# Kernel tuning notes

Hardware: AMD Instinct MI355X
Metric: run time of the kernel (lower is better)

Reference implementation:

```python
import jax, jax.numpy as jnp
import numpy as np

N_HEADS = 16

def setup_inputs() -> dict:
    key = jax.random.key(0)
    ks = jax.random.split(key, 7)
    B, S, D = 2, 2048, 1024
    sc = 0.02
    return {
        "x": jax.random.normal(ks[0], (B, S, D), dtype=jnp.float32),
        "Wq": jax.random.normal(ks[1], (D, D), dtype=jnp.float32) * sc,
        "bq": jax.random.normal(ks[2], (D,), dtype=jnp.float32) * sc,
        "Wk": jax.random.normal(ks[3], (D, D), dtype=jnp.float32) * sc,
        "bk": jax.random.normal(ks[4], (D,), dtype=jnp.float32) * sc,
        "Wv": jax.random.normal(ks[5], (D, D), dtype=jnp.float32) * sc,
        "bv": jax.random.normal(ks[6], (D,), dtype=jnp.float32) * sc,
    }

def reference(x, Wq, bq, Wk, bk, Wv, bv):
    B, S, D = x.shape
    H = N_HEADS
    W = D // H  # head width
    # torch Linear: y = x @ W.T + b
    q = x @ Wq.T + bq
    k = x @ Wk.T + bk
    v = x @ Wv.T + bv
    # split last dim into (H, W) and move heads forward: (B, H, S, W)
    q = q.reshape(B, S, H, W).transpose(0, 2, 1, 3)
    k = k.reshape(B, S, H, W).transpose(0, 2, 1, 3)
    v = v.reshape(B, S, H, W).transpose(0, 2, 1, 3)
    scores = jnp.einsum("bhqw,bhkw->bhqk", q, k) / jnp.sqrt(jnp.asarray(W, x.dtype))
    # original applies softmax, (dropout=identity at eval), then softmax AGAIN
    scores = jax.nn.softmax(scores, axis=-1)
    scores = jax.nn.softmax(scores, axis=-1)
    h = jnp.einsum("bhqk,bhkw->bhqw", scores, v)
    h = h.transpose(0, 2, 1, 3).reshape(B, S, D)
    return h
```

## Files before the change

kernel.cpp:

```cpp
#include <hip/hip_runtime.h>
#include <cstdint>
#include <cstddef>

typedef __bf16 bf16_t;
typedef __bf16 bf16x2 __attribute__((ext_vector_type(2)));
typedef __bf16 bf16x4 __attribute__((ext_vector_type(4)));
typedef __bf16 bf16x8 __attribute__((ext_vector_type(8)));
typedef float f32x4 __attribute__((ext_vector_type(4)));
typedef unsigned int u32x2 __attribute__((ext_vector_type(2)));

typedef __attribute__((address_space(1))) unsigned int gu32;
typedef __attribute__((address_space(3))) unsigned int lu32;

#define MFMA16(a, b, c) __builtin_amdgcn_mfma_f32_16x16x32_bf16((a), (b), (c), 0, 0, 0)

__device__ __forceinline__ void gload_lds16(const void* g, void* l) {
    __builtin_amdgcn_global_load_lds((gu32*)const_cast<void*>(g), (lu32*)l, 16, 0, 0);
}

__global__ __launch_bounds__(256) void cvt_bf16(
    const float* __restrict__ x, const float* __restrict__ Wq,
    const float* __restrict__ Wk, const float* __restrict__ Wv,
    bf16_t* __restrict__ xb, bf16_t* __restrict__ Wqb,
    bf16_t* __restrict__ Wkb, bf16_t* __restrict__ Wvb)
{
    const int z = blockIdx.z;
    const float* src = (z == 0) ? x : (z == 1) ? Wq : (z == 2) ? Wk : Wv;
    bf16_t* dst      = (z == 0) ? xb : (z == 1) ? Wqb : (z == 2) ? Wkb : Wvb;
    const int n = (z == 0) ? 4096 * 1024 : 1024 * 1024;
    const int stride = gridDim.x * blockDim.x * 4;
    for (int i = (blockIdx.x * blockDim.x + threadIdx.x) * 4; i < n; i += stride) {
        const float4 f = *(const float4*)(src + i);
        bf16x4 o; o[0] = (bf16_t)f.x; o[1] = (bf16_t)f.y; o[2] = (bf16_t)f.z; o[3] = (bf16_t)f.w;
        *(bf16x4*)(dst + i) = o;
    }
}

__global__ __launch_bounds__(512) void qkv_gemm_bf16(
    const bf16_t* __restrict__ xb,
    const bf16_t* __restrict__ W0b, const float* __restrict__ b0,
    const bf16_t* __restrict__ W1b, const float* __restrict__ b1,
    const bf16_t* __restrict__ W2b, const float* __restrict__ b2,
    bf16_t* __restrict__ Qo, bf16_t* __restrict__ Ko, bf16_t* __restrict__ VTo,
    float* __restrict__ Vp)
{
    const int z = blockIdx.z;
    const bf16_t* Wm = (z == 0) ? W0b : (z == 1) ? W1b : W2b;
    const float* bia = (z == 0) ? b0 : (z == 1) ? b1 : b2;

    __shared__ bf16_t As[2][128 * 32];
    __shared__ bf16_t Bs[2][128 * 32];

    const int tid  = threadIdx.x;
    const int lane = tid & 63;
    const int wv   = tid >> 6;
    const int quad = lane >> 4;
    const int l16  = lane & 15;
    const int wm   = wv >> 1;
    const int wn   = wv & 1;
    const int m0   = blockIdx.x * 128;
    const int n0   = blockIdx.y * 128;

    const int rs = tid >> 2;
    const int gs = ((tid & 3) ^ ((rs >> 1) & 3)) * 8;
    const int fp = (quad ^ ((l16 >> 1) & 3)) * 8;

    f32x4 acc[2][4];
    for (int i = 0; i < 2; i++)
        for (int j = 0; j < 4; j++) acc[i][j] = (f32x4)0.0f;

    gload_lds16(xb + (size_t)(m0 + rs) * 1024 + gs, &As[0][(wv * 64) * 8]);
    gload_lds16(Wm + (size_t)(n0 + rs) * 1024 + gs, &Bs[0][(wv * 64) * 8]);

#pragma unroll 2
    for (int kt = 0; kt < 32; kt++) {
        const int cur = kt & 1, nxt = cur ^ 1;
        __syncthreads();
        if (kt < 31) {
            const int kp = (kt + 1) * 32;
            gload_lds16(xb + (size_t)(m0 + rs) * 1024 + kp + gs, &As[nxt][(wv * 64) * 8]);
            gload_lds16(Wm + (size_t)(n0 + rs) * 1024 + kp + gs, &Bs[nxt][(wv * 64) * 8]);
        }
        bf16x8 af[2], bfr[4];
        for (int mt = 0; mt < 2; mt++)
            af[mt] = *(const bf16x8*)&As[cur][(wm * 32 + mt * 16 + l16) * 32 + fp];
        for (int nt = 0; nt < 4; nt++)
            bfr[nt] = *(const bf16x8*)&Bs[cur][(wn * 64 + nt * 16 + l16) * 32 + fp];
        for (int mt = 0; mt < 2; mt++)
            for (int nt = 0; nt < 4; nt++)
                acc[mt][nt] = MFMA16(af[mt], bfr[nt], acc[mt][nt]);
    }

    float bv[4];
    for (int nt = 0; nt < 4; nt++)
        bv[nt] = bia[n0 + wn * 64 + nt * 16 + l16];

    if (z < 2) {
        bf16_t* out = (z == 0) ? Qo : Ko;
        const float scl = (z == 0) ? 0.18033688011112042f : 1.0f;
        for (int mt = 0; mt < 2; mt++) {
            const int mrow = m0 + wm * 32 + mt * 16 + quad * 4;
            for (int nt = 0; nt < 4; nt++) {
                const int n = n0 + wn * 64 + nt * 16 + l16;
                for (int r = 0; r < 4; r++)
                    out[(size_t)(mrow + r) * 1024 + n] = (bf16_t)((acc[mt][nt][r] + bv[nt]) * scl);
            }
        }
    } else {
        const int h = blockIdx.y * 2 + wn;
        float psum[4] = {0.f, 0.f, 0.f, 0.f};
        for (int mt = 0; mt < 2; mt++) {
            const int sg = m0 + wm * 32 + mt * 16 + quad * 4;
            const int bb = sg >> 11;
            const int s  = sg & 2047;
            for (int nt = 0; nt < 4; nt++) {
                const int w = nt * 16 + l16;
                bf16x4 pk;
                for (int r = 0; r < 4; r++) {
                    pk[r] = (bf16_t)(acc[mt][nt][r] + bv[nt]);
                    psum[nt] += (float)pk[r];
                }
                *(bf16x4*)(VTo + ((size_t)((bb * 16 + h) * 64 + w)) * 2048 + s) = pk;
            }
        }
        for (int nt = 0; nt < 4; nt++) {
            psum[nt] += __shfl_xor(psum[nt], 16, 64);
            psum[nt] += __shfl_xor(psum[nt], 32, 64);
        }
        float* red = (float*)&As[0][0];
        if (quad == 0)
            for (int nt = 0; nt < 4; nt++)
                red[(wv * 4 + nt) * 16 + l16] = psum[nt];
        __syncthreads();
        if (wm == 0 && quad == 0) {
            const int bb = m0 >> 11;
            const int j  = blockIdx.x & 15;
            for (int nt = 0; nt < 4; nt++) {
                float s4 = ((red[((wn + 0) * 4 + nt) * 16 + l16]
                           + red[((wn + 2) * 4 + nt) * 16 + l16])
                           + red[((wn + 4) * 4 + nt) * 16 + l16])
                           + red[((wn + 6) * 4 + nt) * 16 + l16];
                Vp[((size_t)((bb * 16 + h) * 64 + nt * 16 + l16)) * 16 + j] = s4;
            }
        }
    }
}

__global__ __launch_bounds__(512, 4) void attn(
    const bf16_t* __restrict__ Qg, const bf16_t* __restrict__ Kg,
    const bf16_t* __restrict__ VTg, const float* __restrict__ Vp,
    float* __restrict__ out)
{
    const int qt = blockIdx.x;
    const int h  = blockIdx.y;
    const int b  = blockIdx.z;

    const int tid  = threadIdx.x;
    const int wv   = tid >> 6;
    const int lane = tid & 63;
    const int quad = lane >> 4;
    const int l16  = lane & 15;
    const int qg   = wv >> 1;
    const int sh   = wv & 1;

    const size_t base  = ((size_t)b * 2048) * 1024 + (size_t)h * 64;
    const size_t vbase = ((size_t)(b * 16 + h) * 64) * 2048;
    const int q0 = qt * 128;

    __shared__ __align__(16) unsigned char smem[49152];
    bf16_t* Qs = (bf16_t*)smem;

    {
        const int c0 = tid, c1 = 512 + tid;
        const int r0 = c0 >> 3, g0 = ((c0 & 7) ^ (r0 & 7)) * 8;
        const int r1 = c1 >> 3, g1 = ((c1 & 7) ^ (r1 & 7)) * 8;
        gload_lds16(Qg + base + (size_t)(q0 + r0) * 1024 + g0, Qs + (wv * 64) * 8);
        gload_lds16(Qg + base + (size_t)(q0 + r1) * 1024 + g1, Qs + (512 + wv * 64) * 8);
    }
    const int rk = tid >> 3;
    const int gk = ((tid & 7) ^ (rk & 7)) * 8;
    gload_lds16(Kg + base + (size_t)rk * 1024 + gk,
                (bf16_t*)(smem + 16384) + (wv * 64) * 8);
    gload_lds16(VTg + vbase + (size_t)rk * 2048 + gk,
                (bf16_t*)(smem + 32768) + (wv * 64) * 8);

    const int fs0 = ((0 ^ quad) ^ (l16 & 7)) * 8;
    const int fs1 = ((4 ^ quad) ^ (l16 & 7)) * 8;
    const int fsA = sh ? fs1 : fs0;

    const int qr0 = qg * 32 + l16;
    const int qr1 = qg * 32 + 16 + l16;

    f32x4 oa[2][4], l1acc[2];
    for (int qs = 0; qs < 2; qs++) {
        for (int nt = 0; nt < 4; nt++) oa[qs][nt] = (f32x4)0.0f;
        l1acc[qs] = (f32x4)0.0f;
    }

    bf16x8 ones;
    for (int j = 0; j < 8; j++) ones[j] = (bf16_t)1.0f;

    __syncthreads();

    bf16x8 aq[2][2];
    aq[0][0] = *(const bf16x8*)&Qs[qr0 * 64 + fs0];
    aq[0][1] = *(const bf16x8*)&Qs[qr0 * 64 + fs1];
    aq[1][0] = *(const bf16x8*)&Qs[qr1 * 64 + fs0];
    aq[1][1] = *(const bf16x8*)&Qs[qr1 * 64 + fs1];

    bf16x8 af[2];
    bf16x8 bvf[4];

    #define EXCHANGE_P(PS_SA)                                                   \
        for (int qs = 0; qs < 2; qs++) {                                        \
            union { bf16x2 h; unsigned int u; } t00, t01, t10, t11;             \
            t00.h[0] = (bf16_t)__builtin_amdgcn_exp2f(PS_SA[0][qs][0]);         \
            t00.h[1] = (bf16_t)__builtin_amdgcn_exp2f(PS_SA[0][qs][1]);         \
            t01.h[0] = (bf16_t)__builtin_amdgcn_exp2f(PS_SA[0][qs][2]);         \
            t01.h[1] = (bf16_t)__builtin_amdgcn_exp2f(PS_SA[0][qs][3]);         \
            t10.h[0] = (bf16_t)__builtin_amdgcn_exp2f(PS_SA[1][qs][0]);         \
            t10.h[1] = (bf16_t)__builtin_amdgcn_exp2f(PS_SA[1][qs][1]);         \
            t11.h[0] = (bf16_t)__builtin_amdgcn_exp2f(PS_SA[1][qs][2]);         \
            t11.h[1] = (bf16_t)__builtin_amdgcn_exp2f(PS_SA[1][qs][3]);         \
            u32x2 p0 = __builtin_amdgcn_permlane32_swap(t00.u, t10.u, false, false); \
            u32x2 e0 = __builtin_amdgcn_permlane16_swap(p0[0], p0[1], false, false); \
            u32x2 p1 = __builtin_amdgcn_permlane32_swap(t01.u, t11.u, false, false); \
            u32x2 e1 = __builtin_amdgcn_permlane16_swap(p1[0], p1[1], false, false); \
            union { unsigned int u[4]; bf16x8 h; } w;                           \
            w.u[0] = e0[0]; w.u[1] = e1[0]; w.u[2] = e0[1]; w.u[3] = e1[1];     \
            af[qs] = w.h;                                                       \
        }

    {
        const bf16_t* Ks0 = (const bf16_t*)(smem + 16384);
        const bf16_t* Vs0 = (const bf16_t*)(smem + 32768);
        gload_lds16(Kg + base + (size_t)(64 + rk) * 1024 + gk,
                    (bf16_t*)(smem + 24576) + (wv * 64) * 8);
        gload_lds16(VTg + vbase + (size_t)rk * 2048 + 64 + gk,
                    (bf16_t*)(smem + 40960) + (wv * 64) * 8);

        f32x4 sa[2][2];
        for (int st = 0; st < 2; st++)
            for (int qs = 0; qs < 2; qs++) sa[st][qs] = (f32x4)0.0f;
        for (int st = 0; st < 2; st++) {
            const int srow = (sh * 32 + st * 16 + l16) * 64;
            bf16x8 kb0 = *(const bf16x8*)&Ks0[srow + fs0];
            bf16x8 kb1 = *(const bf16x8*)&Ks0[srow + fs1];
            for (int qs = 0; qs < 2; qs++) {
                sa[st][qs] = MFMA16(kb0, aq[qs][0], sa[st][qs]);
                sa[st][qs] = MFMA16(kb1, aq[qs][1], sa[st][qs]);
            }
        }
        EXCHANGE_P(sa)
        for (int nt = 0; nt < 4; nt++)
            bvf[nt] = *(const bf16x8*)&Vs0[(nt * 16 + l16) * 64 + fsA];
    }

#pragma unroll 2
    for (int kt = 1; kt < 32; kt++) {
        const int cur = kt & 1, prv = cur ^ 1;
        const bf16_t* KsC = (const bf16_t*)(smem + 16384 + cur * 8192);
        const bf16_t* VsC = (const bf16_t*)(smem + 32768 + cur * 8192);
        __syncthreads();

        if (kt < 31) {
            gload_lds16(Kg + base + (size_t)((kt + 1) * 64 + rk) * 1024 + gk,
                        (bf16_t*)(smem + 16384 + prv * 8192) + (wv * 64) * 8);
            gload_lds16(VTg + vbase + (size_t)rk * 2048 + (kt + 1) * 64 + gk,
                        (bf16_t*)(smem + 32768 + prv * 8192) + (wv * 64) * 8);
        }

        f32x4 sa[2][2];
        for (int st = 0; st < 2; st++)
            for (int qs = 0; qs < 2; qs++) sa[st][qs] = (f32x4)0.0f;
        __builtin_amdgcn_s_setprio(1);
        for (int st = 0; st < 2; st++) {
            const int srow = (sh * 32 + st * 16 + l16) * 64;
            bf16x8 kb0 = *(const bf16x8*)&KsC[srow + fs0];
            bf16x8 kb1 = *(const bf16x8*)&KsC[srow + fs1];
            for (int qs = 0; qs < 2; qs++) {
                sa[st][qs] = MFMA16(kb0, aq[qs][0], sa[st][qs]);
                sa[st][qs] = MFMA16(kb1, aq[qs][1], sa[st][qs]);
            }
        }

        l1acc[0] = MFMA16(af[0], ones, l1acc[0]);
        l1acc[1] = MFMA16(af[1], ones, l1acc[1]);
        for (int nt = 0; nt < 4; nt++) {
            oa[0][nt] = MFMA16(af[0], bvf[nt], oa[0][nt]);
            oa[1][nt] = MFMA16(af[1], bvf[nt], oa[1][nt]);
        }
        __builtin_amdgcn_s_setprio(0);

        for (int nt = 0; nt < 4; nt++)
            bvf[nt] = *(const bf16x8*)&VsC[(nt * 16 + l16) * 64 + fsA];

        EXCHANGE_P(sa)
    }

    {
        l1acc[0] = MFMA16(af[0], ones, l1acc[0]);
        l1acc[1] = MFMA16(af[1], ones, l1acc[1]);
        for (int nt = 0; nt < 4; nt++) {
            oa[0][nt] = MFMA16(af[0], bvf[nt], oa[0][nt]);
            oa[1][nt] = MFMA16(af[1], bvf[nt], oa[1][nt]);
        }
    }

    __syncthreads();
    f32x4* R4 = (f32x4*)smem;
    f32x4* L4 = (f32x4*)(smem + 32768);
    const int bi = qg * 64 + lane;
    if (sh == 1) {
        for (int qs = 0; qs < 2; qs++)
            for (int nt = 0; nt < 4; nt++)
                R4[bi * 8 + ((qs * 4 + nt) ^ (lane & 7))] = oa[qs][nt];
        L4[bi * 2 + 0] = l1acc[0];
        L4[bi * 2 + 1] = l1acc[1];
    }
    __syncthreads();
    if (sh == 0) {
        for (int qs = 0; qs < 2; qs++)
            for (int nt = 0; nt < 4; nt++)
                oa[qs][nt] += R4[bi * 8 + ((qs * 4 + nt) ^ (lane & 7))];
        l1acc[0] += L4[bi * 2 + 0];
        l1acc[1] += L4[bi * 2 + 1];

        float invq[2][4];
        for (int qs = 0; qs < 2; qs++)
            for (int r = 0; r < 4; r++) invq[qs][r] = 1.0f / l1acc[qs][r];

        float vs[4];
        const size_t vprow = (size_t)(b * 16 + h) * 64;
        for (int nt = 0; nt < 4; nt++) {
            const f32x4 p4 = *(const f32x4*)&Vp[(vprow + nt * 16 + l16) * 16 + quad * 4];
            float t = (p4[0] + p4[1]) + (p4[2] + p4[3]);
            t += __shfl_xor(t, 16, 64);
            t += __shfl_xor(t, 32, 64);
            vs[nt] = t;
        }

        const float inv_denom = 1.0f / 2049.0f;
        for (int qs = 0; qs < 2; qs++)
            for (int nt = 0; nt < 4; nt++)
                for (int r = 0; r < 4; r++) {
                    const int srow = q0 + qg * 32 + qs * 16 + quad * 4 + r;
                    out[((size_t)b * 2048 + srow) * 1024 + (size_t)h * 64 + nt * 16 + l16] =
                        (vs[nt] + oa[qs][nt][r] * invq[qs][r]) * inv_denom;
                }
    }
    #undef EXCHANGE_P
}

extern "C" void kernel_launch(void* const* d_in, const int* in_sizes, int n_in,
                              void* d_out, int out_size, void* d_ws, size_t ws_size,
                              hipStream_t stream) {
    const float* x  = (const float*)d_in[0];
    const float* Wq = (const float*)d_in[1];
    const float* bq = (const float*)d_in[2];
    const float* Wk = (const float*)d_in[3];
    const float* bk = (const float*)d_in[4];
    const float* Wv = (const float*)d_in[5];
    const float* bv = (const float*)d_in[6];

    bf16_t* Qw  = (bf16_t*)d_ws;
    bf16_t* Kw  = Qw + (size_t)4096 * 1024;
    bf16_t* VTw = Kw + (size_t)4096 * 1024;
    float*  Vp  = (float*)(VTw + (size_t)4096 * 1024);

    bf16_t* xb  = (bf16_t*)d_out;
    bf16_t* Wqb = xb + (size_t)4096 * 1024;
    bf16_t* Wkb = Wqb + (size_t)1024 * 1024;
    bf16_t* Wvb = Wkb + (size_t)1024 * 1024;

    cvt_bf16<<<dim3(1024, 1, 4), 256, 0, stream>>>(x, Wq, Wk, Wv, xb, Wqb, Wkb, Wvb);
    qkv_gemm_bf16<<<dim3(32, 8, 3), 512, 0, stream>>>(
        xb, Wqb, bq, Wkb, bk, Wvb, bv, Qw, Kw, VTw, Vp);
    attn<<<dim3(16, 16, 2), 512, 0, stream>>>(Qw, Kw, VTw, Vp, (float*)d_out);
}
```

Before: 154.7 us.

## Load V fragments directly from global into registers, shrink LDS to 32KB

V^T tiles no longer go through LDS. Each lane loads its MFMA B-operand fragments straight from global memory into two register buffers that alternate between iterations. This cuts shared memory from 48KB to 32KB, which could allow more blocks per CU, and removes the LDS write/read traffic for V. The loop is also reordered so PV runs before the next QK. The risks are higher register pressure and global-load latency exposed in the loop, plus extra barriers at the end because the reduction now reuses the smaller LDS.

Measured after the change: 187.9 us. +21.4%, slower.

```diff
diff --git a/kernel.cpp b/kernel.cpp
--- a/kernel.cpp
+++ b/kernel.cpp
@@ -167,8 +167,13 @@
     const size_t vbase = ((size_t)(b * 16 + h) * 64) * 2048;
     const int q0 = qt * 128;
 
-    __shared__ __align__(16) unsigned char smem[49152];
+    __shared__ __align__(16) unsigned char smem[32768];
     bf16_t* Qs = (bf16_t*)smem;
+
+    const bf16_t* Vg = VTg + vbase + (size_t)l16 * 2048 + sh * 32 + quad * 8;
+    #define VLOAD(B, KT)                                                        \
+        for (int nt = 0; nt < 4; nt++)                                          \
+            B[nt] = *(const bf16x8*)(Vg + (size_t)nt * 32768 + (KT) * 64);
 
     {
         const int c0 = tid, c1 = 512 + tid;
@@ -181,12 +186,12 @@
     const int gk = ((tid & 7) ^ (rk & 7)) * 8;
     gload_lds16(Kg + base + (size_t)rk * 1024 + gk,
                 (bf16_t*)(smem + 16384) + (wv * 64) * 8);
-    gload_lds16(VTg + vbase + (size_t)rk * 2048 + gk,
-                (bf16_t*)(smem + 32768) + (wv * 64) * 8);
+
+    bf16x8 bvf0[4], bvf1[4];
+    VLOAD(bvf0, 0)
 
     const int fs0 = ((0 ^ quad) ^ (l16 & 7)) * 8;
     const int fs1 = ((4 ^ quad) ^ (l16 & 7)) * 8;
-    const int fsA = sh ? fs1 : fs0;
 
     const int qr0 = qg * 32 + l16;
     const int qr1 = qg * 32 + 16 + l16;
@@ -209,7 +214,6 @@
     aq[1][1] = *(const bf16x8*)&Qs[qr1 * 64 + fs1];
 
     bf16x8 af[2];
-    bf16x8 bvf[4];
 
     #define EXCHANGE_P(PS_SA)                                                   \
         for (int qs = 0; qs < 2; qs++) {                                        \
@@ -231,100 +235,90 @@
             af[qs] = w.h;                                                       \
         }
 
+    #define QK_TILE(KSP)                                                        \
+        for (int st = 0; st < 2; st++)                                          \
+            for (int qs = 0; qs < 2; qs++) sa[st][qs] = (f32x4)0.0f;            \
+        for (int st = 0; st < 2; st++) {                                        \
+            const int srow = (sh * 32 + st * 16 + l16) * 64;                    \
+            bf16x8 kb0 = *(const bf16x8*)&(KSP)[srow + fs0];                    \
+            bf16x8 kb1 = *(const bf16x8*)&(KSP)[srow + fs1];                    \
+            for (int qs = 0; qs < 2; qs++) {                                    \
+                sa[st][qs] = MFMA16(kb0, aq[qs][0], sa[st][qs]);                \
+                sa[st][qs] = MFMA16(kb1, aq[qs][1], sa[st][qs]);                \
+            }                                                                   \
+        }
+
+    #define PV_TILE(BPV)                                                        \
+        l1acc[0] = MFMA16(af[0], ones, l1acc[0]);                               \
+        l1acc[1] = MFMA16(af[1], ones, l1acc[1]);                               \
+        for (int nt = 0; nt < 4; nt++) {                                        \
+            oa[0][nt] = MFMA16(af[0], BPV[nt], oa[0][nt]);                      \
+            oa[1][nt] = MFMA16(af[1], BPV[nt], oa[1][nt]);                      \
+        }
+
     {
         const bf16_t* Ks0 = (const bf16_t*)(smem + 16384);
-        const bf16_t* Vs0 = (const bf16_t*)(smem + 32768);
         gload_lds16(Kg + base + (size_t)(64 + rk) * 1024 + gk,
                     (bf16_t*)(smem + 24576) + (wv * 64) * 8);
-        gload_lds16(VTg + vbase + (size_t)rk * 2048 + 64 + gk,
-                    (bf16_t*)(smem + 40960) + (wv * 64) * 8);
-
+        VLOAD(bvf1, 1)
         f32x4 sa[2][2];
-        for (int st = 0; st < 2; st++)
-            for (int qs = 0; qs < 2; qs++) sa[st][qs] = (f32x4)0.0f;
-        for (int st = 0; st < 2; st++) {
-            const int srow = (sh * 32 + st * 16 + l16) * 64;
-            bf16x8 kb0 = *(const bf16x8*)&Ks0[srow + fs0];
-            bf16x8 kb1 = *(const bf16x8*)&Ks0[srow + fs1];
-            for (int qs = 0; qs < 2; qs++) {
-                sa[st][qs] = MFMA16(kb0, aq[qs][0], sa[st][qs]);
-                sa[st][qs] = MFMA16(kb1, aq[qs][1], sa[st][qs]);
-            }
-        }
+        __builtin_amdgcn_s_setprio(1);
+        QK_TILE(Ks0)
+        __builtin_amdgcn_s_setprio(0);
         EXCHANGE_P(sa)
-        for (int nt = 0; nt < 4; nt++)
-            bvf[nt] = *(const bf16x8*)&Vs0[(nt * 16 + l16) * 64 + fsA];
-    }
-
-#pragma unroll 2
-    for (int kt = 1; kt < 32; kt++) {
-        const int cur = kt & 1, prv = cur ^ 1;
-        const bf16_t* KsC = (const bf16_t*)(smem + 16384 + cur * 8192);
-        const bf16_t* VsC = (const bf16_t*)(smem + 32768 + cur * 8192);
-        __syncthreads();
-
-        if (kt < 31) {
-            gload_lds16(Kg + base + (size_t)((kt + 1) * 64 + rk) * 1024 + gk,
-                        (bf16_t*)(smem + 16384 + prv * 8192) + (wv * 64) * 8);
-            gload_lds16(VTg + vbase + (size_t)rk * 2048 + (kt + 1) * 64 + gk,
-                        (bf16_t*)(smem + 32768 + prv * 8192) + (wv * 64) * 8);
-        }
-
-        f32x4 sa[2][2];
-        for (int st = 0; st < 2; st++)
-            for (int qs = 0; qs < 2; qs++) sa[st][qs] = (f32x4)0.0f;
-        __builtin_amdgcn_s_setprio(1);
-        for (int st = 0; st < 2; st++) {
-            const int srow = (sh * 32 + st * 16 + l16) * 64;
-            bf16x8 kb0 = *(const bf16x8*)&KsC[srow + fs0];
-            bf16x8 kb1 = *(const bf16x8*)&KsC[srow + fs1];
-            for (int qs = 0; qs < 2; qs++) {
-                sa[st][qs] = MFMA16(kb0, aq[qs][0], sa[st][qs]);
-                sa[st][qs] = MFMA16(kb1, aq[qs][1], sa[st][qs]);
-            }
-        }
-
-        l1acc[0] = MFMA16(af[0], ones, l1acc[0]);
-        l1acc[1] = MFMA16(af[1], ones, l1acc[1]);
-        for (int nt = 0; nt < 4; nt++) {
-            oa[0][nt] = MFMA16(af[0], bvf[nt], oa[0][nt]);
-            oa[1][nt] = MFMA16(af[1], bvf[nt], oa[1][nt]);
-        }
-        __builtin_amdgcn_s_setprio(0);
-
-        for (int nt = 0; nt < 4; nt++)
-            bvf[nt] = *(const bf16x8*)&VsC[(nt * 16 + l16) * 64 + fsA];
-
-        EXCHANGE_P(sa)
+    }
+
+    #define ITER(KT, BPV)                                                       \
+    {                                                                           \
+        const int cur_ = (KT) & 1, prv_ = cur_ ^ 1;                             \
+        const bf16_t* KsC = (const bf16_t*)(smem + 16384 + cur_ * 8192);        \
+        __syncthreads();                                                        \
+        if ((KT) < 31)                                                          \
+            gload_lds16(Kg + base + (size_t)(((KT) + 1) * 64 + rk) * 1024 + gk, \
+                        (bf16_t*)(smem + 16384 + prv_ * 8192) + (wv * 64) * 8); \
+        f32x4 sa[2][2];                                                         \
+        __builtin_amdgcn_s_setprio(1);                                          \
+        PV_TILE(BPV)                                                            \
+        __builtin_amdgcn_s_setprio(0);                                          \
+        if ((KT) < 31) { VLOAD(BPV, (KT) + 1) }                                 \
+        __builtin_amdgcn_s_setprio(1);                                          \
+        QK_TILE(KsC)                                                            \
+        __builtin_amdgcn_s_setprio(0);                                          \
+        EXCHANGE_P(sa)                                                          \
+    }
+
+    for (int kt = 1; kt < 32; kt += 2) {
+        ITER(kt, bvf0)
+        if (kt + 1 < 32) ITER(kt + 1, bvf1)
     }
 
     {
-        l1acc[0] = MFMA16(af[0], ones, l1acc[0]);
-        l1acc[1] = MFMA16(af[1], ones, l1acc[1]);
-        for (int nt = 0; nt < 4; nt++) {
-            oa[0][nt] = MFMA16(af[0], bvf[nt], oa[0][nt]);
-            oa[1][nt] = MFMA16(af[1], bvf[nt], oa[1][nt]);
-        }
+        PV_TILE(bvf1)
     }
 
     __syncthreads();
     f32x4* R4 = (f32x4*)smem;
-    f32x4* L4 = (f32x4*)(smem + 32768);
     const int bi = qg * 64 + lane;
     if (sh == 1) {
         for (int qs = 0; qs < 2; qs++)
             for (int nt = 0; nt < 4; nt++)
                 R4[bi * 8 + ((qs * 4 + nt) ^ (lane & 7))] = oa[qs][nt];
-        L4[bi * 2 + 0] = l1acc[0];
-        L4[bi * 2 + 1] = l1acc[1];
     }
     __syncthreads();
     if (sh == 0) {
         for (int qs = 0; qs < 2; qs++)
             for (int nt = 0; nt < 4; nt++)
                 oa[qs][nt] += R4[bi * 8 + ((qs * 4 + nt) ^ (lane & 7))];
-        l1acc[0] += L4[bi * 2 + 0];
-        l1acc[1] += L4[bi * 2 + 1];
+    }
+    __syncthreads();
+    if (sh == 1) {
+        R4[bi * 2 + 0] = l1acc[0];
+        R4[bi * 2 + 1] = l1acc[1];
+    }
+    __syncthreads();
+    if (sh == 0) {
+        l1acc[0] += R4[bi * 2 + 0];
+        l1acc[1] += R4[bi * 2 + 1];
 
         float invq[2][4];
         for (int qs = 0; qs < 2; qs++)
@@ -349,7 +343,11 @@
                         (vs[nt] + oa[qs][nt][r] * invq[qs][r]) * inv_denom;
                 }
     }
+    #undef ITER
+    #undef PV_TILE
+    #undef QK_TILE
     #undef EXCHANGE_P
+    #undef VLOAD
 }
 
 extern "C" void kernel_launch(void* const* d_in, const int* in_sizes, int n_in,
```

## Stage K/V tiles in pairs to halve block barriers in attention loop

Applied to the files above, without the earlier changes.

Reworks the K/V LDS staging so each async load batch fetches two 64-key tiles at once into a four-slot ring, and the main loop synchronises only on even iterations instead of every iteration. This aims to cut barrier count and give the global-to-LDS loads more time to land before use. The cost is LDS growth from 48KB to 80KB per block, which can reduce how many blocks fit per CU and so lower occupancy.

After: 157.6 us. About the same (+1.9%).

```diff
diff --git a/kernel.cpp b/kernel.cpp
--- a/kernel.cpp
+++ b/kernel.cpp
@@ -167,8 +167,27 @@
     const size_t vbase = ((size_t)(b * 16 + h) * 64) * 2048;
     const int q0 = qt * 128;
 
-    __shared__ __align__(16) unsigned char smem[49152];
+    __shared__ __align__(16) unsigned char smem[81920];
     bf16_t* Qs = (bf16_t*)smem;
+
+    #define KS(KT) ((bf16_t*)(smem + 16384 + (((KT) >> 1) & 1) * 16384 + ((KT) & 1) * 8192))
+    #define VS(KT) ((bf16_t*)(smem + 49152 + (((KT) >> 1) & 1) * 16384 + ((KT) & 1) * 8192))
+
+    const int rk = tid >> 3;
+    const int gk = ((tid & 7) ^ (rk & 7)) * 8;
+
+    #define STAGE_PAIR(P)                                                       \
+    {                                                                           \
+        const int pr_ = (P) * 128;                                              \
+        gload_lds16(Kg + base + (size_t)(pr_ + rk) * 1024 + gk,                 \
+                    KS(2 * (P)) + (wv * 64) * 8);                               \
+        gload_lds16(Kg + base + (size_t)(pr_ + 64 + rk) * 1024 + gk,            \
+                    KS(2 * (P) + 1) + (wv * 64) * 8);                           \
+        gload_lds16(VTg + vbase + (size_t)rk * 2048 + pr_ + gk,                 \
+                    VS(2 * (P)) + (wv * 64) * 8);                               \
+        gload_lds16(VTg + vbase + (size_t)rk * 2048 + pr_ + 64 + gk,            \
+                    VS(2 * (P) + 1) + (wv * 64) * 8);                           \
+    }
 
     {
         const int c0 = tid, c1 = 512 + tid;
@@ -177,12 +196,7 @@
         gload_lds16(Qg + base + (size_t)(q0 + r0) * 1024 + g0, Qs + (wv * 64) * 8);
         gload_lds16(Qg + base + (size_t)(q0 + r1) * 1024 + g1, Qs + (512 + wv * 64) * 8);
     }
-    const int rk = tid >> 3;
-    const int gk = ((tid & 7) ^ (rk & 7)) * 8;
-    gload_lds16(Kg + base + (size_t)rk * 1024 + gk,
-                (bf16_t*)(smem + 16384) + (wv * 64) * 8);
-    gload_lds16(VTg + vbase + (size_t)rk * 2048 + gk,
-                (bf16_t*)(smem + 32768) + (wv * 64) * 8);
+    STAGE_PAIR(0)
 
     const int fs0 = ((0 ^ quad) ^ (l16 & 7)) * 8;
     const int fs1 = ((4 ^ quad) ^ (l16 & 7)) * 8;
@@ -231,59 +245,44 @@
             af[qs] = w.h;                                                       \
         }
 
+    #define QK_TILE(KSP)                                                        \
+        for (int st = 0; st < 2; st++)                                          \
+            for (int qs = 0; qs < 2; qs++) sa[st][qs] = (f32x4)0.0f;            \
+        for (int st = 0; st < 2; st++) {                                        \
+            const int srow = (sh * 32 + st * 16 + l16) * 64;                    \
+            bf16x8 kb0 = *(const bf16x8*)&(KSP)[srow + fs0];                    \
+            bf16x8 kb1 = *(const bf16x8*)&(KSP)[srow + fs1];                    \
+            for (int qs = 0; qs < 2; qs++) {                                    \
+                sa[st][qs] = MFMA16(kb0, aq[qs][0], sa[st][qs]);                \
+                sa[st][qs] = MFMA16(kb1, aq[qs][1], sa[st][qs]);                \
+            }                                                                   \
+        }
+
     {
-        const bf16_t* Ks0 = (const bf16_t*)(smem + 16384);
-        const bf16_t* Vs0 = (const bf16_t*)(smem + 32768);
-        gload_lds16(Kg + base + (size_t)(64 + rk) * 1024 + gk,
-                    (bf16_t*)(smem + 24576) + (wv * 64) * 8);
-        gload_lds16(VTg + vbase + (size_t)rk * 2048 + 64 + gk,
-                    (bf16_t*)(smem + 40960) + (wv * 64) * 8);
-
+        STAGE_PAIR(1)
         f32x4 sa[2][2];
-        for (int st = 0; st < 2; st++)
-            for (int qs = 0; qs < 2; qs++) sa[st][qs] = (f32x4)0.0f;
-        for (int st = 0; st < 2; st++) {
-            const int srow = (sh * 32 + st * 16 + l16) * 64;
-            bf16x8 kb0 = *(const bf16x8*)&Ks0[srow + fs0];
-            bf16x8 kb1 = *(const bf16x8*)&Ks0[srow + fs1];
-            for (int qs = 0; qs < 2; qs++) {
-                sa[st][qs] = MFMA16(kb0, aq[qs][0], sa[st][qs]);
-                sa[st][qs] = MFMA16(kb1, aq[qs][1], sa[st][qs]);
-            }
-        }
+        __builtin_amdgcn_s_setprio(1);
+        QK_TILE(KS(0))
+        __builtin_amdgcn_s_setprio(0);
         EXCHANGE_P(sa)
         for (int nt = 0; nt < 4; nt++)
-            bvf[nt] = *(const bf16x8*)&Vs0[(nt * 16 + l16) * 64 + fsA];
+            bvf[nt] = *(const bf16x8*)&VS(0)[(nt * 16 + l16) * 64 + fsA];
     }
 
 #pragma unroll 2
     for (int kt = 1; kt < 32; kt++) {
-        const int cur = kt & 1, prv = cur ^ 1;
-        const bf16_t* KsC = (const bf16_t*)(smem + 16384 + cur * 8192);
-        const bf16_t* VsC = (const bf16_t*)(smem + 32768 + cur * 8192);
-        __syncthreads();
-
-        if (kt < 31) {
-            gload_lds16(Kg + base + (size_t)((kt + 1) * 64 + rk) * 1024 + gk,
-                        (bf16_t*)(smem + 16384 + prv * 8192) + (wv * 64) * 8);
-            gload_lds16(VTg + vbase + (size_t)rk * 2048 + (kt + 1) * 64 + gk,
-                        (bf16_t*)(smem + 32768 + prv * 8192) + (wv * 64) * 8);
-        }
+        if ((kt & 1) == 0) {
+            __syncthreads();
+            const int p = (kt >> 1) + 1;
+            if (p < 16) STAGE_PAIR(p)
+        }
+
+        const bf16_t* KsC = KS(kt);
+        const bf16_t* VsC = VS(kt);
 
         f32x4 sa[2][2];
-        for (int st = 0; st < 2; st++)
-            for (int qs = 0; qs < 2; qs++) sa[st][qs] = (f32x4)0.0f;
         __builtin_amdgcn_s_setprio(1);
-        for (int st = 0; st < 2; st++) {
-            const int srow = (sh * 32 + st * 16 + l16) * 64;
-            bf16x8 kb0 = *(const bf16x8*)&KsC[srow + fs0];
-            bf16x8 kb1 = *(const bf16x8*)&KsC[srow + fs1];
-            for (int qs = 0; qs < 2; qs++) {
-                sa[st][qs] = MFMA16(kb0, aq[qs][0], sa[st][qs]);
-                sa[st][qs] = MFMA16(kb1, aq[qs][1], sa[st][qs]);
-            }
-        }
-
+        QK_TILE(KsC)
         l1acc[0] = MFMA16(af[0], ones, l1acc[0]);
         l1acc[1] = MFMA16(af[1], ones, l1acc[1]);
         for (int nt = 0; nt < 4; nt++) {
@@ -349,7 +348,11 @@
                         (vs[nt] + oa[qs][nt][r] * invq[qs][r]) * inv_denom;
                 }
     }
+    #undef QK_TILE
     #undef EXCHANGE_P
+    #undef STAGE_PAIR
+    #undef VS
+    #undef KS
 }
 
 extern "C" void kernel_launch(void* const* d_in, const int* in_sizes, int n_in,
```
